# Performance work log

Hardware: AMD Instinct MI355X
Metric: run time of the kernel (lower is better)

## Reference

```python
import jax, jax.numpy as jnp
import numpy as np

N_HEADS = 8
DIM_HEAD = 64
SCALE = DIM_HEAD ** -0.5


def setup_inputs() -> dict:
    key = jax.random.key(0)
    ks = jax.random.split(key, 7)
    B, C, H, W = 2, 512, 64, 64
    inner = N_HEADS * DIM_HEAD  # 512
    x = jax.random.normal(ks[0], (B, C, H, W), dtype=jnp.float32)
    context = jax.random.normal(ks[1], (B, C, H, W), dtype=jnp.float32)
    # kaiming_normal fan_out for 1x1 conv: std = sqrt(2 / out_channels)
    std_qkv = (2.0 / inner) ** 0.5
    std_o = (2.0 / C) ** 0.5
    Wq = jax.random.normal(ks[2], (inner, C), dtype=jnp.float32) * std_qkv
    Wk = jax.random.normal(ks[3], (inner, C), dtype=jnp.float32) * std_qkv
    Wv = jax.random.normal(ks[4], (inner, C), dtype=jnp.float32) * std_qkv
    Wo = jax.random.normal(ks[5], (C, inner), dtype=jnp.float32) * std_o
    return {
        'x': x, 'context': context,
        'Wq': Wq, 'bq': jnp.zeros((inner,), jnp.float32),
        'Wk': Wk, 'bk': jnp.zeros((inner,), jnp.float32),
        'Wv': Wv, 'bv': jnp.zeros((inner,), jnp.float32),
        'Wo': Wo, 'bo': jnp.zeros((C,), jnp.float32),
    }


def _attention(x, context, Wq, bq, Wk, bk, Wv, bv, Wo, bo):
    b, c, h, w = x.shape
    s = h * w
    # 1x1 conv == per-pixel channel matmul. Flatten spatial: [b, s, c]
    xf = x.reshape(b, c, s).transpose(0, 2, 1)
    cf = context.reshape(b, c, s).transpose(0, 2, 1)
    q = jnp.einsum('bsc,ec->bse', xf, Wq) + bq  # [b, s, inner]
    k = jnp.einsum('bsc,ec->bse', cf, Wk) + bk
    v = jnp.einsum('bsc,ec->bse', cf, Wv) + bv
    # split heads: [b, n, s, d]
    def split(t):
        return t.reshape(b, s, N_HEADS, DIM_HEAD).transpose(0, 2, 1, 3)
    q, k, v = split(q), split(k), split(v)
    sim = jnp.einsum('bnid,bnjd->bnij', q, k) * SCALE  # [b, n, s, s]
    attn = jax.nn.softmax(sim, axis=-1)
    out = jnp.einsum('bnij,bnjd->bnid', attn, v)  # [b, n, s, d]
    # merge heads back to channels: 'b n s d -> b (n d) s'
    out = out.transpose(0, 2, 1, 3).reshape(b, s, N_HEADS * DIM_HEAD)
    out = jnp.einsum('bse,ce->bsc', out, Wo) + bo  # output proj (1x1 conv)
    return out.transpose(0, 2, 1).reshape(b, c, h, w)


def reference(x, context, Wq, bq, Wk, bk, Wv, bv, Wo, bo):
    return _attention(x, context, Wq, bq, Wk, bk, Wv, bv, Wo, bo)
```

## Files before the change

### kernel.cpp

```cpp
#include <hip/hip_runtime.h>
#include <cstdint>


typedef __bf16 bf16x8 __attribute__((ext_vector_type(8)));
typedef __bf16 bf16x4 __attribute__((ext_vector_type(4)));
typedef float f32x4 __attribute__((ext_vector_type(4)));
typedef unsigned short u16x8 __attribute__((ext_vector_type(8)));
typedef unsigned short u16x4 __attribute__((ext_vector_type(4)));

#define AS1 __attribute__((address_space(1)))
#define AS3 __attribute__((address_space(3)))

__device__ __forceinline__ void async16(const void* g, void* l) {
  __builtin_amdgcn_global_load_lds((const AS1 void*)g, (AS3 void*)l, 16, 0, 0);
}

__device__ __forceinline__ uint16_t f2bf(float f) {
  union { float f; uint32_t u; } a;
  a.f = f;
  uint32_t r = a.u + 0x7fffu + ((a.u >> 16) & 1u);
  return (uint16_t)(r >> 16);
}

__device__ __forceinline__ float bf2f(uint16_t u) {
  union { uint32_t u; float f; } a;
  a.u = (uint32_t)u << 16;
  return a.f;
}

__global__ __launch_bounds__(256) void prep(
    const float* __restrict__ x, const float* __restrict__ ctx,
    const float* __restrict__ Wq, const float* __restrict__ Wk,
    const float* __restrict__ Wv, const float* __restrict__ Wo,
    uint16_t* __restrict__ xT, uint16_t* __restrict__ cT,
    uint16_t* __restrict__ Wqb, uint16_t* __restrict__ Wkb,
    uint16_t* __restrict__ Wvb, uint16_t* __restrict__ Wob) {
  const int zz = blockIdx.z;
  const int t = threadIdx.x;
  if (zz == 4) {
    const float* W[4] = {Wq, Wk, Wv, Wo};
    uint16_t* O[4] = {Wqb, Wkb, Wvb, Wob};
    const int blk = blockIdx.x + 64 * blockIdx.y;
    const size_t base = (size_t)blk * 2048 + (size_t)t * 8;
    const int w = (int)(base >> 18);
    const size_t off = base & 262143;
    float4 v0 = *(const float4*)&W[w][off];
    float4 v1 = *(const float4*)&W[w][off + 4];
    u16x8 o = {f2bf(v0.x), f2bf(v0.y), f2bf(v0.z), f2bf(v0.w),
               f2bf(v1.x), f2bf(v1.y), f2bf(v1.z), f2bf(v1.w)};
    *(u16x8*)&O[w][off] = o;
    return;
  }
  const float* src = (zz < 2 ? x : ctx) + (size_t)(zz & 1) * 512 * 4096;
  uint16_t* dst = (zz < 2 ? xT : cT) + (size_t)(zz & 1) * 4096 * 512;
  const int s0 = blockIdx.x * 64, c0 = blockIdx.y * 64;
  __shared__ uint16_t tile[64][80];
  for (int p = 0; p < 2; ++p) {
    int u = p * 256 + t;
    int r = u >> 3, cg = (u & 7) * 8;
    const float* sp = &src[(size_t)(c0 + r) * 4096 + s0 + cg];
    float4 v0 = *(const float4*)sp;
    float4 v1 = *(const float4*)(sp + 4);
    u16x8 o = {f2bf(v0.x), f2bf(v0.y), f2bf(v0.z), f2bf(v0.w),
               f2bf(v1.x), f2bf(v1.y), f2bf(v1.z), f2bf(v1.w)};
    *(u16x8*)&tile[r][cg] = o;
  }
  __syncthreads();
  for (int p = 0; p < 2; ++p) {
    int u = p * 256 + t;
    int sr = u >> 3, cg = (u & 7) * 8;
    u16x8 v;
    for (int j = 0; j < 8; ++j) v[j] = tile[cg + j][sr];
    *(u16x8*)&dst[(size_t)(s0 + sr) * 512 + c0 + cg] = v;
  }
}

struct QkvArgs {
  const uint16_t* A[3]; long long sA[3];
  const uint16_t* B[3]; long long sB[3];
  uint16_t* C[3];       long long sC[3];
  const float* bias[3];
  float os[3];
  long long ldC[3]; int lx[3]; int brow[3];
};

__global__ __launch_bounds__(256) void gemm_qkv(QkvArgs ga) {
  constexpr int K = 512;
  __shared__ uint16_t At[128 * 32];
  __shared__ uint16_t Bt[128 * 32];
  const int t = threadIdx.x, lane = t & 63, wave = t >> 6;
  const int lr = lane & 15, lq = lane >> 4;
  const int wm = (wave >> 1) * 64, wn = (wave & 1) * 64;
  const int sel = blockIdx.z >> 1, bat = blockIdx.z & 1;
  const int lx = ga.lx[sel], brow = ga.brow[sel];
  const long long ldC = ga.ldC[sel];
  const float os = ga.os[sel];
  const int n0 = (blockIdx.x & ((1 << lx) - 1)) * 128;
  const int m0 = (blockIdx.x >> lx) * 128;
  const uint16_t* A = ga.A[sel] + (size_t)bat * ga.sA[sel];
  const uint16_t* B = ga.B[sel] + (size_t)bat * ga.sB[sel];
  const float* bias = ga.bias[sel];
  f32x4 acc[4][4] = {};
  for (int k0 = 0; k0 < K; k0 += 32) {
    __syncthreads();
    for (int p = 0; p < 2; ++p) {
      int u = p * 256 + t;
      int r = u >> 2, c = (u & 3) * 8;
      async16(&A[(size_t)(m0 + r) * K + k0 + c], &At[p * 2048 + wave * 512]);
      async16(&B[(size_t)(n0 + r) * K + k0 + c], &Bt[p * 2048 + wave * 512]);
    }
    __builtin_amdgcn_s_waitcnt(0);
    __syncthreads();
    bf16x8 af[4], bfr[4];
    for (int i = 0; i < 4; ++i)
      af[i] = *(const bf16x8*)&At[(wm + i * 16 + lr) * 32 + lq * 8];
    for (int j = 0; j < 4; ++j)
      bfr[j] = *(const bf16x8*)&Bt[(wn + j * 16 + lr) * 32 + lq * 8];
    for (int i = 0; i < 4; ++i)
      for (int j = 0; j < 4; ++j)
        acc[i][j] = __builtin_amdgcn_mfma_f32_16x16x32_bf16(af[i], bfr[j], acc[i][j], 0, 0, 0);
  }
  uint16_t* C = ga.C[sel] + (size_t)bat * ga.sC[sel];
  for (int i = 0; i < 4; ++i)
    for (int j = 0; j < 4; ++j) {
      int row = m0 + wm + i * 16 + lq * 4;
      int col = n0 + wn + j * 16 + lr;
      float bc = brow ? 0.f : bias[col];
      u16x4 o;
      for (int r = 0; r < 4; ++r) {
        float val = (acc[i][j][r] + (brow ? bias[row + r] : bc)) * os;
        o[r] = f2bf(val);
      }
      *(u16x4*)&C[(size_t)col * ldC + row] = o;
    }
}

__global__ __launch_bounds__(256) void gemm_out(
    const uint16_t* __restrict__ Ap, const float* __restrict__ Lp,
    const uint16_t* __restrict__ Wo, float* __restrict__ Y,
    const float* __restrict__ bias) {
  constexpr int K = 512, S = 4096, E = 512;
  __shared__ uint16_t At[128 * 32];
  __shared__ uint16_t Bt[64 * 32];
  const int t = threadIdx.x, lane = t & 63, wave = t >> 6;
  const int lr = lane & 15, lq = lane >> 4;
  const int wm = (wave & 1) * 64, wn = (wave >> 1) * 32;
  const int m0 = blockIdx.y * 128, n0 = blockIdx.x * 64;
  const int b = blockIdx.z;
  const size_t bOff = (size_t)b * S * E;
  const size_t HALF = (size_t)2 * S * E;
  f32x4 acc[4][2] = {};
  for (int k0 = 0; k0 < K; k0 += 32) {
    const int h = k0 >> 6;
    const float* l0p = &Lp[((size_t)b * 8 + h) * S];
    const float* l1p = &Lp[((size_t)(2 + b) * 8 + h) * S];
    __syncthreads();
    for (int p = 0; p < 2; ++p) {
      int u = p * 256 + t;
      int r = u >> 2, c = (u & 3) * 8;
      size_t off = bOff + (size_t)(m0 + r) * E + k0 + c;
      u16x4 a00 = *(const u16x4*)&Ap[off];
      u16x4 a01 = *(const u16x4*)&Ap[off + 4];
      u16x4 a10 = *(const u16x4*)&Ap[HALF + off];
      u16x4 a11 = *(const u16x4*)&Ap[HALF + off + 4];
      float inv = 1.f / (l0p[m0 + r] + l1p[m0 + r]);
      u16x8 o;
      for (int q = 0; q < 4; ++q) {
        o[q]     = f2bf((bf2f(a00[q]) + bf2f(a10[q])) * inv);
        o[q + 4] = f2bf((bf2f(a01[q]) + bf2f(a11[q])) * inv);
      }
      *(u16x8*)&At[r * 32 + c] = o;
    }
    {
      int r = t >> 2, c = (t & 3) * 8;
      async16(&Wo[(size_t)(n0 + r) * K + k0 + c], &Bt[wave * 512]);
    }
    __builtin_amdgcn_s_waitcnt(0);
    __syncthreads();
    bf16x8 af[4], bfr[2];
    for (int i = 0; i < 4; ++i)
      af[i] = *(const bf16x8*)&At[(wm + i * 16 + lr) * 32 + lq * 8];
    for (int j = 0; j < 2; ++j)
      bfr[j] = *(const bf16x8*)&Bt[(wn + j * 16 + lr) * 32 + lq * 8];
    for (int i = 0; i < 4; ++i)
      for (int j = 0; j < 2; ++j)
        acc[i][j] = __builtin_amdgcn_mfma_f32_16x16x32_bf16(af[i], bfr[j], acc[i][j], 0, 0, 0);
  }
  float* Cf = Y + (size_t)b * 512 * 4096;
  for (int i = 0; i < 4; ++i)
    for (int j = 0; j < 2; ++j) {
      int row = m0 + wm + i * 16 + lq * 4;
      int col = n0 + wn + j * 16 + lr;
      float bb = bias[col];
      float4 o = {acc[i][j][0] + bb, acc[i][j][1] + bb,
                  acc[i][j][2] + bb, acc[i][j][3] + bb};
      *(float4*)&Cf[(size_t)col * 4096 + row] = o;
    }
}

__global__ __launch_bounds__(512, 4) void attn128(
    const uint16_t* __restrict__ Q, const uint16_t* __restrict__ K,
    const uint16_t* __restrict__ Vt, uint16_t* __restrict__ Ap,
    float* __restrict__ Lp) {
  constexpr int S = 4096, E = 512;
  const int b = blockIdx.z & 1, jh = blockIdx.z >> 1;
  const int h = blockIdx.y;
  const int i0 = blockIdx.x * 256;
  const int t = threadIdx.x, lane = t & 63, wave = t >> 6;
  const int lr = lane & 15, lq = lane >> 4;
  const size_t qkB = (size_t)b * S * E;
  const size_t vB = (size_t)b * E * S;
  __shared__ uint16_t Kl[2][64 * 64];
  __shared__ uint16_t Vl[2][64 * 64];
  __shared__ __bf16 Pl[8 * 2 * 16 * 72];

  const int qbase = i0 + wave * 32;
  bf16x8 qf[2][2];
  for (int g = 0; g < 2; ++g) {
    const size_t qo = qkB + (size_t)(qbase + g * 16 + lr) * E + h * 64 + lq * 8;
    qf[g][0] = *(const bf16x8*)&Q[qo];
    qf[g][1] = *(const bf16x8*)&Q[qo + 32];
  }
  f32x4 lsum[2] = {};
  f32x4 accOT[2][4] = {};
  const int swz = (lr & 7);
  const int srr = t >> 3, ssc = ((t & 7) ^ (srr & 7)) * 8;

  const int jbeg = jh * (S / 2), jend = jbeg + S / 2;
  async16(&K[qkB + (size_t)(jbeg + srr) * E + h * 64 + ssc], &Kl[0][wave * 512]);
  async16(&Vt[vB + (size_t)(h * 64 + srr) * S + jbeg + ssc], &Vl[0][wave * 512]);
  __builtin_amdgcn_s_waitcnt(0);
  __syncthreads();

  int cur = 0;
  for (int j0 = jbeg; j0 < jend; j0 += 64) {
    if (j0 + 64 < jend) {
      async16(&K[qkB + (size_t)(j0 + 64 + srr) * E + h * 64 + ssc], &Kl[cur ^ 1][wave * 512]);
      async16(&Vt[vB + (size_t)(h * 64 + srr) * S + j0 + 64 + ssc], &Vl[cur ^ 1][wave * 512]);
    }
    const uint16_t* Kc = Kl[cur];
    const uint16_t* Vc = Vl[cur];
    f32x4 svt[2][4];
    for (int jn = 0; jn < 4; ++jn) {
      const int row = jn * 16 + lr;
      const int c0 = (lq ^ swz) * 8;
      bf16x8 ka0 = *(const bf16x8*)&Kc[row * 64 + c0];
      bf16x8 ka1 = *(const bf16x8*)&Kc[row * 64 + (c0 ^ 32)];
      for (int g = 0; g < 2; ++g) {
        f32x4 z = {0.f, 0.f, 0.f, 0.f};
        z = __builtin_amdgcn_mfma_f32_16x16x32_bf16(ka0, qf[g][0], z, 0, 0, 0);
        z = __builtin_amdgcn_mfma_f32_16x16x32_bf16(ka1, qf[g][1], z, 0, 0, 0);
        svt[g][jn] = z;
      }
    }
    for (int g = 0; g < 2; ++g) {
      __bf16* pr = &Pl[((wave * 2 + g) * 16 + lr) * 72];
      for (int jn = 0; jn < 4; ++jn) {
        f32x4 p;
        for (int r = 0; r < 4; ++r) p[r] = exp2f(svt[g][jn][r]);
        lsum[g] += p;
        bf16x4 pk;
        for (int r = 0; r < 4; ++r) pk[r] = (__bf16)p[r];
        *(bf16x4*)&pr[jn * 16 + lq * 4] = pk;
      }
    }
    bf16x8 pa[2][2];
    for (int g = 0; g < 2; ++g) {
      const __bf16* pr = &Pl[((wave * 2 + g) * 16 + lr) * 72];
      pa[g][0] = *(const bf16x8*)&pr[lq * 8];
      pa[g][1] = *(const bf16x8*)&pr[32 + lq * 8];
    }
    for (int dn = 0; dn < 4; ++dn) {
      const int row = dn * 16 + lr;
      const int c0 = (lq ^ swz) * 8;
      bf16x8 v0 = *(const bf16x8*)&Vc[row * 64 + c0];
      bf16x8 v1 = *(const bf16x8*)&Vc[row * 64 + (c0 ^ 32)];
      for (int g = 0; g < 2; ++g) {
        accOT[g][dn] = __builtin_amdgcn_mfma_f32_16x16x32_bf16(v0, pa[g][0], accOT[g][dn], 0, 0, 0);
        accOT[g][dn] = __builtin_amdgcn_mfma_f32_16x16x32_bf16(v1, pa[g][1], accOT[g][dn], 0, 0, 0);
      }
    }
    __builtin_amdgcn_s_waitcnt(0);
    __syncthreads();
    cur ^= 1;
  }
  uint16_t* Aph = Ap + (size_t)jh * 2 * S * E;
  float* Lph = Lp + ((size_t)(jh * 2 + b) * 8 + h) * S;
  for (int g = 0; g < 2; ++g) {
    float lt = (lsum[g][0] + lsum[g][1]) + (lsum[g][2] + lsum[g][3]);
    lt += __shfl_xor(lt, 16);
    lt += __shfl_xor(lt, 32);
    if (lane < 16) Lph[qbase + g * 16 + lr] = lt;
    const size_t row = qbase + g * 16 + lr;
    for (int dn = 0; dn < 4; ++dn) {
      u16x4 o;
      for (int r = 0; r < 4; ++r) o[r] = f2bf(accOT[g][dn][r]);
      *(u16x4*)&Aph[qkB + row * E + h * 64 + dn * 16 + lq * 4] = o;
    }
  }
}

extern "C" void kernel_launch(void* const* d_in, const int* in_sizes, int n_in,
                              void* d_out, int out_size, void* d_ws, size_t ws_size,
                              hipStream_t stream) {
  const float* x   = (const float*)d_in[0];
  const float* ctx = (const float*)d_in[1];
  const float* Wq  = (const float*)d_in[2];
  const float* bq  = (const float*)d_in[3];
  const float* Wk  = (const float*)d_in[4];
  const float* bk  = (const float*)d_in[5];
  const float* Wv  = (const float*)d_in[6];
  const float* bv  = (const float*)d_in[7];
  const float* Wo  = (const float*)d_in[8];
  const float* bo  = (const float*)d_in[9];
  float* out = (float*)d_out;

  const size_t SZ = (size_t)2 * 4096 * 512;
  uint16_t* xT = (uint16_t*)d_ws;
  uint16_t* cT = xT + SZ;
  uint16_t* Qb = cT + SZ;
  uint16_t* Kb = Qb + SZ;
  uint16_t* Vb = Kb + SZ;
  uint16_t* Wqb = Vb + SZ;
  uint16_t* Wkb = Wqb + 512 * 512;
  uint16_t* Wvb = Wkb + 512 * 512;
  uint16_t* Wob = Wvb + 512 * 512;
  uint16_t* Ap  = Wob + 512 * 512;
  float*    Lp  = (float*)(Ap + 2 * SZ);
  const long long sIn = 4096LL * 512LL;
  const float slh = 0.125f * 1.44269504088896f;

  prep<<<dim3(64, 8, 5), 256, 0, stream>>>(x, ctx, Wq, Wk, Wv, Wo,
                                           xT, cT, Wqb, Wkb, Wvb, Wob);
  QkvArgs qkv = {
      {Wqb, Wkb, cT}, {0, 0, sIn},
      {xT, cT, Wvb}, {sIn, sIn, 0},
      {Qb, Kb, Vb}, {sIn, sIn, sIn},
      {bq, bk, bv},
      {slh, 1.f, 1.f},
      {512, 512, 4096},
      {5, 5, 2},
      {1, 1, 0}};
  gemm_qkv<<<dim3(128, 1, 6), 256, 0, stream>>>(qkv);
  attn128<<<dim3(16, 8, 4), 512, 0, stream>>>(Qb, Kb, Vb, Ap, Lp);
  gemm_out<<<dim3(8, 32, 2), 256, 0, stream>>>(Ap, Lp, Wob, out, bo);
}
```

Baseline: 251.4 us.

## Split attention keys three ways and drop LDS double buffering for occupancy

The attention kernel now splits the key range into three chunks (22/21/21 tiles) instead of two, launching 768 blocks instead of 512 so more CUs have work. The K/V LDS tiles become single-buffered with a barrier before and after each load, which halves shared memory and raises the launch-bounds occupancy hint from 4 to 6. The output GEMM now sums three partial outputs and three partial row sums using wider 8-element loads. In exchange the kernel loses its load/compute overlap, the output GEMM reads more partial data, and the workspace grows.

Result: slower. 505.7 us (+101.2%).

```diff
diff --git a/kernel.cpp b/kernel.cpp
--- a/kernel.cpp
+++ b/kernel.cpp
@@ -152,23 +152,21 @@
   f32x4 acc[4][2] = {};
   for (int k0 = 0; k0 < K; k0 += 32) {
     const int h = k0 >> 6;
-    const float* l0p = &Lp[((size_t)b * 8 + h) * S];
+    const float* l0p = &Lp[((size_t)(0 + b) * 8 + h) * S];
     const float* l1p = &Lp[((size_t)(2 + b) * 8 + h) * S];
+    const float* l2p = &Lp[((size_t)(4 + b) * 8 + h) * S];
     __syncthreads();
     for (int p = 0; p < 2; ++p) {
       int u = p * 256 + t;
       int r = u >> 2, c = (u & 3) * 8;
       size_t off = bOff + (size_t)(m0 + r) * E + k0 + c;
-      u16x4 a00 = *(const u16x4*)&Ap[off];
-      u16x4 a01 = *(const u16x4*)&Ap[off + 4];
-      u16x4 a10 = *(const u16x4*)&Ap[HALF + off];
-      u16x4 a11 = *(const u16x4*)&Ap[HALF + off + 4];
-      float inv = 1.f / (l0p[m0 + r] + l1p[m0 + r]);
+      u16x8 a0 = *(const u16x8*)&Ap[off];
+      u16x8 a1 = *(const u16x8*)&Ap[HALF + off];
+      u16x8 a2 = *(const u16x8*)&Ap[2 * HALF + off];
+      float inv = 1.f / (l0p[m0 + r] + l1p[m0 + r] + l2p[m0 + r]);
       u16x8 o;
-      for (int q = 0; q < 4; ++q) {
-        o[q]     = f2bf((bf2f(a00[q]) + bf2f(a10[q])) * inv);
-        o[q + 4] = f2bf((bf2f(a01[q]) + bf2f(a11[q])) * inv);
-      }
+      for (int q = 0; q < 8; ++q)
+        o[q] = f2bf((bf2f(a0[q]) + bf2f(a1[q]) + bf2f(a2[q])) * inv);
       *(u16x8*)&At[r * 32 + c] = o;
     }
     {
@@ -198,7 +196,7 @@
     }
 }
 
-__global__ __launch_bounds__(512, 4) void attn128(
+__global__ __launch_bounds__(512, 6) void attn128(
     const uint16_t* __restrict__ Q, const uint16_t* __restrict__ K,
     const uint16_t* __restrict__ Vt, uint16_t* __restrict__ Ap,
     float* __restrict__ Lp) {
@@ -210,8 +208,8 @@
   const int lr = lane & 15, lq = lane >> 4;
   const size_t qkB = (size_t)b * S * E;
   const size_t vB = (size_t)b * E * S;
-  __shared__ uint16_t Kl[2][64 * 64];
-  __shared__ uint16_t Vl[2][64 * 64];
+  __shared__ uint16_t Kl[64 * 64];
+  __shared__ uint16_t Vl[64 * 64];
   __shared__ __bf16 Pl[8 * 2 * 16 * 72];
 
   const int qbase = i0 + wave * 32;
@@ -226,26 +224,22 @@
   const int swz = (lr & 7);
   const int srr = t >> 3, ssc = ((t & 7) ^ (srr & 7)) * 8;
 
-  const int jbeg = jh * (S / 2), jend = jbeg + S / 2;
-  async16(&K[qkB + (size_t)(jbeg + srr) * E + h * 64 + ssc], &Kl[0][wave * 512]);
-  async16(&Vt[vB + (size_t)(h * 64 + srr) * S + jbeg + ssc], &Vl[0][wave * 512]);
-  __builtin_amdgcn_s_waitcnt(0);
-  __syncthreads();
-
-  int cur = 0;
+  const int t0 = (jh == 0) ? 0 : (jh == 1) ? 22 : 43;
+  const int tc = (jh == 0) ? 22 : 21;
+  const int jbeg = t0 * 64, jend = (t0 + tc) * 64;
+
   for (int j0 = jbeg; j0 < jend; j0 += 64) {
-    if (j0 + 64 < jend) {
-      async16(&K[qkB + (size_t)(j0 + 64 + srr) * E + h * 64 + ssc], &Kl[cur ^ 1][wave * 512]);
-      async16(&Vt[vB + (size_t)(h * 64 + srr) * S + j0 + 64 + ssc], &Vl[cur ^ 1][wave * 512]);
-    }
-    const uint16_t* Kc = Kl[cur];
-    const uint16_t* Vc = Vl[cur];
+    __syncthreads();
+    async16(&K[qkB + (size_t)(j0 + srr) * E + h * 64 + ssc], &Kl[wave * 512]);
+    async16(&Vt[vB + (size_t)(h * 64 + srr) * S + j0 + ssc], &Vl[wave * 512]);
+    __builtin_amdgcn_s_waitcnt(0);
+    __syncthreads();
     f32x4 svt[2][4];
     for (int jn = 0; jn < 4; ++jn) {
       const int row = jn * 16 + lr;
       const int c0 = (lq ^ swz) * 8;
-      bf16x8 ka0 = *(const bf16x8*)&Kc[row * 64 + c0];
-      bf16x8 ka1 = *(const bf16x8*)&Kc[row * 64 + (c0 ^ 32)];
+      bf16x8 ka0 = *(const bf16x8*)&Kl[row * 64 + c0];
+      bf16x8 ka1 = *(const bf16x8*)&Kl[row * 64 + (c0 ^ 32)];
       for (int g = 0; g < 2; ++g) {
         f32x4 z = {0.f, 0.f, 0.f, 0.f};
         z = __builtin_amdgcn_mfma_f32_16x16x32_bf16(ka0, qf[g][0], z, 0, 0, 0);
@@ -273,16 +267,13 @@
     for (int dn = 0; dn < 4; ++dn) {
       const int row = dn * 16 + lr;
       const int c0 = (lq ^ swz) * 8;
-      bf16x8 v0 = *(const bf16x8*)&Vc[row * 64 + c0];
-      bf16x8 v1 = *(const bf16x8*)&Vc[row * 64 + (c0 ^ 32)];
+      bf16x8 v0 = *(const bf16x8*)&Vl[row * 64 + c0];
+      bf16x8 v1 = *(const bf16x8*)&Vl[row * 64 + (c0 ^ 32)];
       for (int g = 0; g < 2; ++g) {
         accOT[g][dn] = __builtin_amdgcn_mfma_f32_16x16x32_bf16(v0, pa[g][0], accOT[g][dn], 0, 0, 0);
         accOT[g][dn] = __builtin_amdgcn_mfma_f32_16x16x32_bf16(v1, pa[g][1], accOT[g][dn], 0, 0, 0);
       }
     }
-    __builtin_amdgcn_s_waitcnt(0);
-    __syncthreads();
-    cur ^= 1;
   }
   uint16_t* Aph = Ap + (size_t)jh * 2 * S * E;
   float* Lph = Lp + ((size_t)(jh * 2 + b) * 8 + h) * S;
@@ -326,7 +317,7 @@
   uint16_t* Wvb = Wkb + 512 * 512;
   uint16_t* Wob = Wvb + 512 * 512;
   uint16_t* Ap  = Wob + 512 * 512;
-  float*    Lp  = (float*)(Ap + 2 * SZ);
+  float*    Lp  = (float*)(Ap + 3 * SZ);
   const long long sIn = 4096LL * 512LL;
   const float slh = 0.125f * 1.44269504088896f;
 
@@ -342,6 +333,6 @@
       {5, 5, 2},
       {1, 1, 0}};
   gemm_qkv<<<dim3(128, 1, 6), 256, 0, stream>>>(qkv);
-  attn128<<<dim3(16, 8, 4), 512, 0, stream>>>(Qb, Kb, Vb, Ap, Lp);
+  attn128<<<dim3(16, 8, 6), 512, 0, stream>>>(Qb, Kb, Vb, Ap, Lp);
   gemm_out<<<dim3(8, 32, 2), 256, 0, stream>>>(Ap, Lp, Wob, out, bo);
 }
```

## Load K directly into registers, compute row sums via MFMA, widen gemm_out loads

Applied to the files above, without the earlier changes.

The attention kernel stops staging K tiles in LDS. Each wave now loads its K fragments straight from global memory into registers and prefetches the next tile during the QK MFMAs. The softmax denominator is now accumulated with an MFMA against a vector of ones over the bf16 probabilities, replacing the per-element adds and the final cross-lane shuffles. This removes LDS traffic and VALU work, but uses more registers and makes the sum come from bf16-rounded probabilities. In gemm_out, two 8-byte loads per operand are merged into one 16-byte load.

New measurement: 330.7 us. 1.32x slower.

```diff
diff --git a/kernel.cpp b/kernel.cpp
--- a/kernel.cpp
+++ b/kernel.cpp
@@ -152,23 +152,19 @@
   f32x4 acc[4][2] = {};
   for (int k0 = 0; k0 < K; k0 += 32) {
     const int h = k0 >> 6;
-    const float* l0p = &Lp[((size_t)b * 8 + h) * S];
+    const float* l0p = &Lp[((size_t)(0 + b) * 8 + h) * S];
     const float* l1p = &Lp[((size_t)(2 + b) * 8 + h) * S];
     __syncthreads();
     for (int p = 0; p < 2; ++p) {
       int u = p * 256 + t;
       int r = u >> 2, c = (u & 3) * 8;
       size_t off = bOff + (size_t)(m0 + r) * E + k0 + c;
-      u16x4 a00 = *(const u16x4*)&Ap[off];
-      u16x4 a01 = *(const u16x4*)&Ap[off + 4];
-      u16x4 a10 = *(const u16x4*)&Ap[HALF + off];
-      u16x4 a11 = *(const u16x4*)&Ap[HALF + off + 4];
+      u16x8 a0 = *(const u16x8*)&Ap[off];
+      u16x8 a1 = *(const u16x8*)&Ap[HALF + off];
       float inv = 1.f / (l0p[m0 + r] + l1p[m0 + r]);
       u16x8 o;
-      for (int q = 0; q < 4; ++q) {
-        o[q]     = f2bf((bf2f(a00[q]) + bf2f(a10[q])) * inv);
-        o[q + 4] = f2bf((bf2f(a01[q]) + bf2f(a11[q])) * inv);
-      }
+      for (int q = 0; q < 8; ++q)
+        o[q] = f2bf((bf2f(a0[q]) + bf2f(a1[q])) * inv);
       *(u16x8*)&At[r * 32 + c] = o;
     }
     {
@@ -210,7 +206,6 @@
   const int lr = lane & 15, lq = lane >> 4;
   const size_t qkB = (size_t)b * S * E;
   const size_t vB = (size_t)b * E * S;
-  __shared__ uint16_t Kl[2][64 * 64];
   __shared__ uint16_t Vl[2][64 * 64];
   __shared__ __bf16 Pl[8 * 2 * 16 * 72];
 
@@ -221,36 +216,43 @@
     qf[g][0] = *(const bf16x8*)&Q[qo];
     qf[g][1] = *(const bf16x8*)&Q[qo + 32];
   }
-  f32x4 lsum[2] = {};
+  bf16x8 ones;
+  for (int i = 0; i < 8; ++i) ones[i] = (__bf16)1.0f;
+  f32x4 lacc[2] = {};
   f32x4 accOT[2][4] = {};
   const int swz = (lr & 7);
   const int srr = t >> 3, ssc = ((t & 7) ^ (srr & 7)) * 8;
 
   const int jbeg = jh * (S / 2), jend = jbeg + S / 2;
-  async16(&K[qkB + (size_t)(jbeg + srr) * E + h * 64 + ssc], &Kl[0][wave * 512]);
+  const uint16_t* Kb_ = &K[qkB + (size_t)(jbeg + lr) * E + h * 64 + lq * 8];
+
   async16(&Vt[vB + (size_t)(h * 64 + srr) * S + jbeg + ssc], &Vl[0][wave * 512]);
+  bf16x8 ka[4][2];
+  for (int jn = 0; jn < 4; ++jn) {
+    ka[jn][0] = *(const bf16x8*)&Kb_[(size_t)(jn * 16) * E];
+    ka[jn][1] = *(const bf16x8*)&Kb_[(size_t)(jn * 16) * E + 32];
+  }
   __builtin_amdgcn_s_waitcnt(0);
   __syncthreads();
 
   int cur = 0;
   for (int j0 = jbeg; j0 < jend; j0 += 64) {
-    if (j0 + 64 < jend) {
-      async16(&K[qkB + (size_t)(j0 + 64 + srr) * E + h * 64 + ssc], &Kl[cur ^ 1][wave * 512]);
+    const bool more = (j0 + 64 < jend);
+    if (more)
       async16(&Vt[vB + (size_t)(h * 64 + srr) * S + j0 + 64 + ssc], &Vl[cur ^ 1][wave * 512]);
-    }
-    const uint16_t* Kc = Kl[cur];
-    const uint16_t* Vc = Vl[cur];
     f32x4 svt[2][4];
-    for (int jn = 0; jn < 4; ++jn) {
-      const int row = jn * 16 + lr;
-      const int c0 = (lq ^ swz) * 8;
-      bf16x8 ka0 = *(const bf16x8*)&Kc[row * 64 + c0];
-      bf16x8 ka1 = *(const bf16x8*)&Kc[row * 64 + (c0 ^ 32)];
+    for (int jn = 0; jn < 4; ++jn)
       for (int g = 0; g < 2; ++g) {
         f32x4 z = {0.f, 0.f, 0.f, 0.f};
-        z = __builtin_amdgcn_mfma_f32_16x16x32_bf16(ka0, qf[g][0], z, 0, 0, 0);
-        z = __builtin_amdgcn_mfma_f32_16x16x32_bf16(ka1, qf[g][1], z, 0, 0, 0);
+        z = __builtin_amdgcn_mfma_f32_16x16x32_bf16(ka[jn][0], qf[g][0], z, 0, 0, 0);
+        z = __builtin_amdgcn_mfma_f32_16x16x32_bf16(ka[jn][1], qf[g][1], z, 0, 0, 0);
         svt[g][jn] = z;
+      }
+    if (more) {
+      const uint16_t* Kn = Kb_ + (size_t)(j0 + 64 - jbeg) * E;
+      for (int jn = 0; jn < 4; ++jn) {
+        ka[jn][0] = *(const bf16x8*)&Kn[(size_t)(jn * 16) * E];
+        ka[jn][1] = *(const bf16x8*)&Kn[(size_t)(jn * 16) * E + 32];
       }
     }
     for (int g = 0; g < 2; ++g) {
@@ -258,7 +260,6 @@
       for (int jn = 0; jn < 4; ++jn) {
         f32x4 p;
         for (int r = 0; r < 4; ++r) p[r] = exp2f(svt[g][jn][r]);
-        lsum[g] += p;
         bf16x4 pk;
         for (int r = 0; r < 4; ++r) pk[r] = (__bf16)p[r];
         *(bf16x4*)&pr[jn * 16 + lq * 4] = pk;
@@ -273,13 +274,17 @@
     for (int dn = 0; dn < 4; ++dn) {
       const int row = dn * 16 + lr;
       const int c0 = (lq ^ swz) * 8;
-      bf16x8 v0 = *(const bf16x8*)&Vc[row * 64 + c0];
-      bf16x8 v1 = *(const bf16x8*)&Vc[row * 64 + (c0 ^ 32)];
+      bf16x8 v0 = *(const bf16x8*)&Vl[cur][row * 64 + c0];
+      bf16x8 v1 = *(const bf16x8*)&Vl[cur][row * 64 + (c0 ^ 32)];
       for (int g = 0; g < 2; ++g) {
         accOT[g][dn] = __builtin_amdgcn_mfma_f32_16x16x32_bf16(v0, pa[g][0], accOT[g][dn], 0, 0, 0);
         accOT[g][dn] = __builtin_amdgcn_mfma_f32_16x16x32_bf16(v1, pa[g][1], accOT[g][dn], 0, 0, 0);
       }
     }
+    for (int g = 0; g < 2; ++g) {
+      lacc[g] = __builtin_amdgcn_mfma_f32_16x16x32_bf16(ones, pa[g][0], lacc[g], 0, 0, 0);
+      lacc[g] = __builtin_amdgcn_mfma_f32_16x16x32_bf16(ones, pa[g][1], lacc[g], 0, 0, 0);
+    }
     __builtin_amdgcn_s_waitcnt(0);
     __syncthreads();
     cur ^= 1;
@@ -287,10 +292,7 @@
   uint16_t* Aph = Ap + (size_t)jh * 2 * S * E;
   float* Lph = Lp + ((size_t)(jh * 2 + b) * 8 + h) * S;
   for (int g = 0; g < 2; ++g) {
-    float lt = (lsum[g][0] + lsum[g][1]) + (lsum[g][2] + lsum[g][3]);
-    lt += __shfl_xor(lt, 16);
-    lt += __shfl_xor(lt, 32);
-    if (lane < 16) Lph[qbase + g * 16 + lr] = lt;
+    if (lane < 16) Lph[qbase + g * 16 + lr] = lacc[g][0];
     const size_t row = qbase + g * 16 + lr;
     for (int dn = 0; dn < 4; ++dn) {
       u16x4 o;
```
